# Kernel optimization log

Hardware: AMD Instinct MI355X
Metric: run time of the kernel (lower is better)

Reference implementation:

```python
import jax, jax.numpy as jnp
import numpy as np

B, S, D, N, NC = 2, 1024, 1024, 8192, 8


def _srw_chunked(x, h, emb_norm, tau_offset, w_read, w_write, n_chunks):
    Bd, Sd, Dd = x.shape
    Nd = emb_norm.shape[0]
    cs = Nd // n_chunks
    h_bf = h.astype(jnp.bfloat16)
    x_bf = x.astype(jnp.bfloat16)
    emb_bf = emb_norm.astype(jnp.bfloat16)
    read_bf = w_read.astype(jnp.bfloat16)
    write_bf = w_write.astype(jnp.bfloat16)
    z1 = jnp.zeros((Bd, Sd, 1))

    @jax.checkpoint
    def estimate_stats(h, emb, nc_val):
        ec0 = jax.lax.dynamic_slice_in_dim(emb, 0, cs, axis=0)
        sc0 = h @ ec0.T
        s_sum = sc0.sum(axis=-1, keepdims=True).astype(jnp.float32) * nc_val
        sq_sum = (sc0 ** 2).sum(axis=-1, keepdims=True).astype(jnp.float32) * nc_val
        return (s_sum, sq_sum)

    s_sum, sq_sum = estimate_stats(h_bf, emb_bf, n_chunks)
    s_mean = s_sum / Nd
    s_std = jnp.sqrt(sq_sum / Nd - s_mean ** 2) + 1e-08
    tau = s_mean + tau_offset * s_std
    tau_bf = tau.astype(jnp.bfloat16)

    @jax.checkpoint
    def gsrw_step(carry, i):
        out, es, em, ac, lbs, lbq = carry
        s = i * cs
        ec = jax.lax.dynamic_slice_in_dim(emb_bf, s, cs, axis=0)
        rc = jax.lax.dynamic_slice_in_dim(read_bf, s, cs, axis=0)
        wc = jax.lax.dynamic_slice_in_dim(write_bf, s, cs, axis=0)
        sc = h_bf @ ec.T  # [B,S,cs]
        raw = sc - tau_bf
        gc = jnp.where(raw > 0, raw, (1e-06 * jnp.exp(jnp.clip(raw.astype(jnp.float32), -10.0, 0.0))).astype(jnp.bfloat16))
        gc = jnp.clip(gc, 0.0, 10.0)
        eg = (jnp.exp(gc.astype(jnp.float32)) - 1.0).astype(jnp.bfloat16)
        ef = eg.astype(jnp.float32)
        xr = x_bf @ rc.T  # [B,S,cs]
        co = ((eg * xr) @ wc).astype(jnp.float32)  # [B,S,D]
        gn = ef.mean(axis=(0, 1))
        lbs = lbs + gn.sum()
        lbq = lbq + (gn ** 2).sum()
        return ((out + co,
                 es + ef.sum(axis=-1, keepdims=True),
                 jnp.maximum(em, ef.max(axis=-1, keepdims=True)),
                 ac + (raw > 0).sum(axis=-1, keepdims=True).astype(jnp.float32),
                 lbs, lbq), None)

    z_scalar = jnp.float32(0.0)
    init = (jnp.zeros((Bd, Sd, Dd), dtype=jnp.float32), z1,
            jnp.full((Bd, Sd, 1), -1000000000.0), z1, z_scalar, z_scalar)
    (raw_out, tes, tem, tac, lb_sum, lb_sq), _ = jax.lax.scan(gsrw_step, init, jnp.arange(n_chunks))
    inv_es = (1.0 / (tes + 1e-08)).astype(jnp.bfloat16)
    gs = jnp.tanh(tem).astype(jnp.bfloat16)
    out = raw_out * inv_es * gs
    exp_sum_scalar = tes.mean() + 1e-08
    norm_lb_sum = lb_sum / exp_sum_scalar
    norm_lb_sq = lb_sq / exp_sum_scalar ** 2
    lb_loss = norm_lb_sq * Nd - 2.0 * norm_lb_sum + 1.0
    gs_mean = jnp.tanh(tem).mean()
    es_mean = tes.mean()
    return (out.astype(jnp.float32), tac / Nd, tem, lb_loss, gs_mean, es_mean)


def setup_inputs() -> dict:
    key = jax.random.key(0)
    k = jax.random.split(key, 6)
    x = jax.random.normal(k[0], (B, S, D), jnp.float32)
    h = jax.random.normal(k[1], (B, S, D), jnp.float32)
    emb = jax.random.normal(k[2], (N, D), jnp.float32) * 0.02
    w_read = jax.random.normal(k[3], (N, D), jnp.float32) * 0.02
    w_write = jax.random.normal(k[4], (N, D), jnp.float32) * 0.02
    tau_offset = jax.random.normal(k[5], (B, S, 1), jnp.float32) * 0.1
    return {"x": x, "h": h, "emb": emb, "tau_offset": tau_offset,
            "w_read": w_read, "w_write": w_write, "n_chunks": NC}


def reference(x, h, emb, tau_offset, w_read, w_write, n_chunks):
    # caller (_know_forward) unit-normalizes the embedding pool first
    emb_norm = emb / (jnp.linalg.norm(emb, axis=-1, keepdims=True) + 1e-08)
    out, active_frac, gate_max, lb_loss, gs_mean, es_mean = _srw_chunked(
        x, h, emb_norm, tau_offset, w_read, w_write, n_chunks)
    return out
```

## Files before the change

kernel.cpp:

```cpp
#include <hip/hip_runtime.h>


#define MDIM 2048
#define DDIM 1024
#define NDIM 8192

typedef __attribute__((ext_vector_type(8))) __bf16 bf16x8;
typedef __attribute__((ext_vector_type(4))) float f32x4;

static __device__ __forceinline__ unsigned short f2b(float f) {
  unsigned u = __float_as_uint(f);
  u = (u + 0x7FFFu + ((u >> 16) & 1u)) >> 16;
  return (unsigned short)u;
}
static __device__ __forceinline__ float b2f(unsigned short s) {
  return __uint_as_float(((unsigned)s) << 16);
}

#define LDSF(off) (*(const bf16x8*)(lds + (off)))
#define MFMA_BF16 __builtin_amdgcn_mfma_f32_16x16x32_bf16

#define GLOAD_LDS(gp, lp)                                                              \
  __builtin_amdgcn_global_load_lds(                                                    \
      (const __attribute__((address_space(1))) unsigned int*)(const void*)(gp),        \
      (__attribute__((address_space(3))) unsigned int*)(void*)(lp), 16, 0, 0)

static __device__ __forceinline__ void stage_half(const unsigned short* __restrict__ src,
                                                  int ld, int row0, int k0,
                                                  char* lds, int lds_off, int w, int l) {
  const int rsub = l >> 3;
  const int col = k0 + 8 * ((l & 7) ^ rsub);
#pragma unroll
  for (int j = 0; j < 2; ++j) {
    const unsigned short* g =
        src + (size_t)(row0 + w * 8 + j * 64 + rsub) * (size_t)ld + col;
    GLOAD_LDS(g, lds + lds_off + j * 8192 + w * 1024);
  }
}

static __device__ __forceinline__ void stage4(const unsigned short* __restrict__ asrc,
                                              const unsigned short* __restrict__ bsrc,
                                              int ld, int m0, int n0, int k0,
                                              char* lds, int buf, int w, int l) {
  stage_half(asrc, ld, m0,       k0, lds, buf,         w, l);
  stage_half(asrc, ld, m0 + 128, k0, lds, buf + 16384, w, l);
  stage_half(bsrc, ld, n0,       k0, lds, buf + 32768, w, l);
  stage_half(bsrc, ld, n0 + 128, k0, lds, buf + 49152, w, l);
}

static __device__ __forceinline__ void gemm256(const unsigned short* __restrict__ asrc,
                                               const unsigned short* __restrict__ bsrc,
                                               int ld, int m0, int n0, int kbase,
                                               char* lds, f32x4 (&acc)[8][4],
                                               int w, int l, int wr, int wc) {
  const int lrow = l & 15, lk = l >> 4;
  const int axor = (l & 7) << 4;
  const int kx0 = (lk << 4) ^ axor;
  const int kx1 = (64 | (lk << 4)) ^ axor;
  const int arow_off = lrow * 128;
  const int brow_off = ((wc & 1) * 64 + lrow) * 128;

  stage4(asrc, bsrc, ld, m0, n0, kbase, lds, 0, w, l);
  asm volatile("s_waitcnt vmcnt(0)" ::: "memory");
  __builtin_amdgcn_s_barrier();

#pragma unroll 1
  for (int t = 0; t < 16; ++t) {
    const int buf = (t & 1) * 65536;
    const int nbuf = 65536 - buf;
    if (t < 15) stage4(asrc, bsrc, ld, m0, n0, kbase + (t + 1) * 64, lds, nbuf, w, l);

    const int ab = buf + wr * 16384;
    const int bb = buf + 32768 + (wc >> 1) * 16384;
    bf16x8 aLO[4][2], aHI[4][2], bLO[2][2], bHI[2][2];
#pragma unroll
    for (int m = 0; m < 4; ++m) {
      aLO[m][0] = LDSF(ab + arow_off + m * 2048 + kx0);
      aLO[m][1] = LDSF(ab + arow_off + m * 2048 + kx1);
    }
#pragma unroll
    for (int n = 0; n < 2; ++n) {
      bLO[n][0] = LDSF(bb + brow_off + n * 2048 + kx0);
      bLO[n][1] = LDSF(bb + brow_off + n * 2048 + kx1);
      bHI[n][0] = LDSF(bb + brow_off + (n + 2) * 2048 + kx0);
      bHI[n][1] = LDSF(bb + brow_off + (n + 2) * 2048 + kx1);
    }
    asm volatile("s_waitcnt lgkmcnt(0)" ::: "memory");
    __builtin_amdgcn_s_setprio(1);
#pragma unroll
    for (int ks = 0; ks < 2; ++ks)
#pragma unroll
      for (int n = 0; n < 2; ++n)
#pragma unroll
        for (int m = 0; m < 4; ++m)
          acc[m][n] = MFMA_BF16(aLO[m][ks], bLO[n][ks], acc[m][n], 0, 0, 0);
    __builtin_amdgcn_s_setprio(0);
#pragma unroll
    for (int m = 0; m < 4; ++m) {
      aHI[m][0] = LDSF(ab + arow_off + (m + 4) * 2048 + kx0);
      aHI[m][1] = LDSF(ab + arow_off + (m + 4) * 2048 + kx1);
    }
    __builtin_amdgcn_s_setprio(1);
#pragma unroll
    for (int ks = 0; ks < 2; ++ks)
#pragma unroll
      for (int n = 0; n < 2; ++n)
#pragma unroll
        for (int m = 0; m < 4; ++m)
          acc[m][n + 2] = MFMA_BF16(aLO[m][ks], bHI[n][ks], acc[m][n + 2], 0, 0, 0);
    __builtin_amdgcn_s_setprio(0);
    asm volatile("s_waitcnt lgkmcnt(0)" ::: "memory");
    __builtin_amdgcn_s_setprio(1);
#pragma unroll
    for (int ks = 0; ks < 2; ++ks)
#pragma unroll
      for (int n = 0; n < 2; ++n)
#pragma unroll
        for (int m = 0; m < 4; ++m)
          acc[m + 4][n + 2] = MFMA_BF16(aHI[m][ks], bHI[n][ks], acc[m + 4][n + 2], 0, 0, 0);
#pragma unroll
    for (int ks = 0; ks < 2; ++ks)
#pragma unroll
      for (int n = 0; n < 2; ++n)
#pragma unroll
        for (int m = 0; m < 4; ++m)
          acc[m + 4][n] = MFMA_BF16(aHI[m][ks], bLO[n][ks], acc[m + 4][n], 0, 0, 0);
    __builtin_amdgcn_s_setprio(0);
    asm volatile("s_waitcnt vmcnt(0)" ::: "memory");
    __builtin_amdgcn_s_barrier();
  }
}


__global__ __launch_bounds__(256) void k_prep(const float* __restrict__ emb,
                                              const float* __restrict__ w_read,
                                              const float* __restrict__ h,
                                              const float* __restrict__ x,
                                              const float* __restrict__ w_write,
                                              unsigned short* __restrict__ eb,
                                              unsigned short* __restrict__ rb,
                                              unsigned short* __restrict__ hb,
                                              unsigned short* __restrict__ xb,
                                              unsigned short* __restrict__ wbT) {
  const int b = blockIdx.x, t = threadIdx.x;
  if (b < 2048) {
    __shared__ float tsm[64][65];
    const int nb = b & 127, db = b >> 7;
    const int r = t >> 2, c4 = (t & 3) * 16;
#pragma unroll
    for (int j = 0; j < 4; ++j) {
      const float4 v = *(const float4*)&w_write[(size_t)(nb * 64 + r) * 1024 + db * 64 + c4 + 4 * j];
      tsm[r][c4 + 4 * j + 0] = v.x;
      tsm[r][c4 + 4 * j + 1] = v.y;
      tsm[r][c4 + 4 * j + 2] = v.z;
      tsm[r][c4 + 4 * j + 3] = v.w;
    }
    __syncthreads();
    const int dr = t >> 2, nc0 = (t & 3) * 16;
    unsigned pk[8];
#pragma unroll
    for (int j = 0; j < 8; ++j) {
      const unsigned lo = f2b(tsm[nc0 + 2 * j][dr]);
      const unsigned hi = f2b(tsm[nc0 + 2 * j + 1][dr]);
      pk[j] = lo | (hi << 16);
    }
    uint4* dst = (uint4*)(wbT + (size_t)(db * 64 + dr) * 8192 + nb * 64 + nc0);
    uint4 w0, w1;
    w0.x = pk[0]; w0.y = pk[1]; w0.z = pk[2]; w0.w = pk[3];
    w1.x = pk[4]; w1.y = pk[5]; w1.z = pk[6]; w1.w = pk[7];
    dst[0] = w0;
    dst[1] = w1;
  } else if (b < 10240) {
    const int n = b - 2048;
    const float4 v = ((const float4*)(emb + (size_t)n * 1024))[t];
    float ss = v.x * v.x + v.y * v.y + v.z * v.z + v.w * v.w;
#pragma unroll
    for (int off = 1; off < 64; off <<= 1) ss += __shfl_xor(ss, off, 64);
    __shared__ float wsum[4];
    if ((t & 63) == 0) wsum[t >> 6] = ss;
    __syncthreads();
    const float denom = sqrtf(wsum[0] + wsum[1] + wsum[2] + wsum[3]) + 1e-8f;
    ushort4 o;
    o.x = f2b(v.x / denom);
    o.y = f2b(v.y / denom);
    o.z = f2b(v.z / denom);
    o.w = f2b(v.w / denom);
    ((ushort4*)(eb + (size_t)n * 1024))[t] = o;
  } else {
    const float* src;
    unsigned short* dst;
    int i;
    if (b < 18432) { src = w_read; dst = rb; i = (b - 10240) * 256 + t; }
    else if (b < 20480) { src = h; dst = hb; i = (b - 18432) * 256 + t; }
    else { src = x; dst = xb; i = (b - 20480) * 256 + t; }
    const float4 v = ((const float4*)src)[i];
    ushort4 o;
    o.x = f2b(v.x);
    o.y = f2b(v.y);
    o.z = f2b(v.z);
    o.w = f2b(v.w);
    ((ushort4*)dst)[i] = o;
  }
}


template <int TROWS>
static __device__ __forceinline__ void stage_tile(const unsigned short* __restrict__ src,
                                                  int row0, int k0, int ld,
                                                  unsigned short* lds, int wave, int lane) {
  const int rsub = lane >> 3;
  const int csub = (lane & 7) << 3;
#pragma unroll
  for (int q = 0; q < TROWS / 32; ++q) {
    const int p = q * 4 + wave;
    const unsigned short* g =
        src + (size_t)(row0 + p * 8 + rsub) * (size_t)ld + (size_t)(k0 + csub);
    GLOAD_LDS(g, lds + p * 512);
  }
}

__global__ __launch_bounds__(256, 2) void k_stats(const unsigned short* __restrict__ hb,
                                                  const unsigned short* __restrict__ eb,
                                                  float* __restrict__ stat_s,
                                                  float* __restrict__ stat_q) {
  __shared__ unsigned short a_sm[64 * 64];
  __shared__ unsigned short b_sm[128 * 64];
  __shared__ float red_s[2][64];
  __shared__ float red_q[2][64];
  const int t = threadIdx.x;
  const int wave = t >> 6, lane = t & 63;
  const int wr = wave >> 1, wc = wave & 1;
  const int m0 = blockIdx.x * 64, n0 = blockIdx.y * 128;
  const int arow = lane & 15;
  const int kcol = (lane >> 4) << 3;
  f32x4 acc[2][4];
#pragma unroll
  for (int m = 0; m < 2; ++m)
#pragma unroll
    for (int n = 0; n < 4; ++n) acc[m][n] = (f32x4)0.0f;
  for (int k0 = 0; k0 < 1024; k0 += 64) {
    stage_tile<64>(hb, m0, k0, 1024, a_sm, wave, lane);
    stage_tile<128>(eb, n0, k0, 1024, b_sm, wave, lane);
    asm volatile("s_waitcnt vmcnt(0)" ::: "memory");
    __syncthreads();
#pragma unroll
    for (int ks = 0; ks < 2; ++ks) {
      bf16x8 af[2], bfr[4];
#pragma unroll
      for (int m = 0; m < 2; ++m)
        af[m] = *(const bf16x8*)&a_sm[(wr * 32 + m * 16 + arow) * 64 + ks * 32 + kcol];
#pragma unroll
      for (int n = 0; n < 4; ++n)
        bfr[n] = *(const bf16x8*)&b_sm[(wc * 64 + n * 16 + arow) * 64 + ks * 32 + kcol];
#pragma unroll
      for (int m = 0; m < 2; ++m)
#pragma unroll
        for (int n = 0; n < 4; ++n)
          acc[m][n] = MFMA_BF16(af[m], bfr[n], acc[m][n], 0, 0, 0);
    }
    __syncthreads();
  }

  float s_r[2][4], q_r[2][4];
#pragma unroll
  for (int m = 0; m < 2; ++m)
#pragma unroll
    for (int i = 0; i < 4; ++i) { s_r[m][i] = 0.f; q_r[m][i] = 0.f; }
#pragma unroll
  for (int m = 0; m < 2; ++m)
#pragma unroll
    for (int n = 0; n < 4; ++n)
#pragma unroll
      for (int i = 0; i < 4; ++i) {
        const float scf = b2f(f2b(acc[m][n][i]));
        s_r[m][i] += scf;
        q_r[m][i] += b2f(f2b(scf * scf));
      }
#pragma unroll
  for (int m = 0; m < 2; ++m)
#pragma unroll
    for (int i = 0; i < 4; ++i) {
      float s = s_r[m][i], q = q_r[m][i];
      for (int off = 1; off < 16; off <<= 1) {
        s += __shfl_xor(s, off, 64);
        q += __shfl_xor(q, off, 64);
      }
      if ((lane & 15) == 0) {
        const int rloc = wr * 32 + m * 16 + (lane >> 4) * 4 + i;
        red_s[wc][rloc] = s;
        red_q[wc][rloc] = q;
      }
    }
  __syncthreads();
  if (t < 64) {
    stat_s[(size_t)(m0 + t) * 8 + blockIdx.y] = red_s[0][t] + red_s[1][t];
    stat_q[(size_t)(m0 + t) * 8 + blockIdx.y] = red_q[0][t] + red_q[1][t];
  }
}

__global__ void k_tau(const float* __restrict__ stat_s, const float* __restrict__ stat_q,
                      const float* __restrict__ tau_off, float* __restrict__ tau) {
  const int r = blockIdx.x * 256 + threadIdx.x;
  if (r >= MDIM) return;
  float S = 0.f, Q = 0.f;
#pragma unroll
  for (int j = 0; j < 8; ++j) {
    S += stat_s[(size_t)r * 8 + j];
    Q += stat_q[(size_t)r * 8 + j];
  }
  const float s_sum = S * 8.0f;
  const float sq_sum = Q * 8.0f;
  const float mean = s_sum * (1.0f / 8192.0f);
  const float var = __fsub_rn(sq_sum * (1.0f / 8192.0f), __fmul_rn(mean, mean));
  const float sd = __fadd_rn(__fsqrt_rn(var), 1e-8f);
  const float tv = __fadd_rn(mean, __fmul_rn(tau_off[r], sd));
  tau[r] = b2f(f2b(tv));
}


__global__ __launch_bounds__(512, 2) void k_sc(const unsigned short* __restrict__ hb,
                                               const unsigned short* __restrict__ eb,
                                               const float* __restrict__ tau,
                                               unsigned short* __restrict__ Aeg,
                                               float* __restrict__ es_part,
                                               float* __restrict__ em_part) {
  __shared__ __align__(16) char lds[131072];
  const int t = threadIdx.x, w = t >> 6, l = t & 63;
  const int wr = w >> 2, wc = w & 3;
  const int bid = blockIdx.x;
  const int swz = (bid & 7) * 32 + (bid >> 3);
  const int m0 = (swz >> 5) * 256, n0 = (swz & 31) * 256;
  f32x4 acc[8][4];
#pragma unroll
  for (int m = 0; m < 8; ++m)
#pragma unroll
    for (int n = 0; n < 4; ++n) acc[m][n] = (f32x4)0.0f;
  gemm256(hb, eb, 1024, m0, n0, 0, lds, acc, w, l, wr, wc);

  __syncthreads();
  float* tau_sm = (float*)lds;
  float* red_es = (float*)(lds + 1024);
  float* red_em = (float*)(lds + 1024 + 4096);
  if (t < 256) tau_sm[t] = tau[m0 + t];
  __syncthreads();
  const int lrow = l & 15, lk = l >> 4;
#pragma unroll
  for (int m = 0; m < 8; ++m) {
#pragma unroll
    for (int i = 0; i < 4; ++i) {
      const int rl = wr * 128 + m * 16 + lk * 4 + i;
      const float taub = tau_sm[rl];
      float es_v = 0.f, em_v = 0.f;
#pragma unroll
      for (int n = 0; n < 4; ++n) {
        const float scf = b2f(f2b(acc[m][n][i]));
        const float rawf = b2f(f2b(scf - taub));
        float gcf;
        if (rawf > 0.f) gcf = fminf(rawf, 10.0f);
        else gcf = b2f(f2b(1e-6f * expf(fmaxf(rawf, -10.0f))));
        const unsigned short egu = f2b(expf(gcf) - 1.0f);
        const float ef = b2f(egu);
        es_v += ef;
        em_v = fmaxf(em_v, ef);
        Aeg[(size_t)(m0 + rl) * NDIM + (size_t)(n0 + wc * 64 + n * 16 + lrow)] = egu;
      }
      for (int off = 1; off < 16; off <<= 1) {
        es_v += __shfl_xor(es_v, off, 64);
        em_v = fmaxf(em_v, __shfl_xor(em_v, off, 64));
      }
      if (lrow == 0) {
        red_es[wc * 256 + rl] = es_v;
        red_em[wc * 256 + rl] = em_v;
      }
    }
  }
  __syncthreads();
  if (t < 256) {
    const float s = red_es[t] + red_es[256 + t] + red_es[512 + t] + red_es[768 + t];
    const float e = fmaxf(fmaxf(red_em[t], red_em[256 + t]),
                          fmaxf(red_em[512 + t], red_em[768 + t]));
    es_part[(size_t)(m0 + t) * 32 + (n0 >> 8)] = s;
    em_part[(size_t)(m0 + t) * 32 + (n0 >> 8)] = e;
  }
}


__global__ __launch_bounds__(512, 2) void k_xr(const unsigned short* __restrict__ xb,
                                               const unsigned short* __restrict__ rb,
                                               unsigned short* __restrict__ Aeg) {
  __shared__ __align__(16) char lds[131072];
  const int t = threadIdx.x, w = t >> 6, l = t & 63;
  const int wr = w >> 2, wc = w & 3;
  const int bid = blockIdx.x;
  const int swz = (bid & 7) * 32 + (bid >> 3);
  const int m0 = (swz >> 5) * 256, n0 = (swz & 31) * 256;
  f32x4 acc[8][4];
#pragma unroll
  for (int m = 0; m < 8; ++m)
#pragma unroll
    for (int n = 0; n < 4; ++n) acc[m][n] = (f32x4)0.0f;
  gemm256(xb, rb, 1024, m0, n0, 0, lds, acc, w, l, wr, wc);

  const int lrow = l & 15, lk = l >> 4;
#pragma unroll
  for (int m = 0; m < 8; ++m)
#pragma unroll
    for (int n = 0; n < 4; ++n)
#pragma unroll
      for (int i = 0; i < 4; ++i) {
        const int rl = wr * 128 + m * 16 + lk * 4 + i;
        const size_t idx =
            (size_t)(m0 + rl) * NDIM + (size_t)(n0 + wc * 64 + n * 16 + lrow);
        const unsigned short egu = Aeg[idx];
        const float xrf = b2f(f2b(acc[m][n][i]));
        Aeg[idx] = f2b(b2f(egu) * xrf);
      }
}


__global__ __launch_bounds__(512, 2) void k_out(const unsigned short* __restrict__ A,
                                                const unsigned short* __restrict__ wbT,
                                                unsigned short* __restrict__ pacc) {
  __shared__ __align__(16) char lds[131072];
  const int t = threadIdx.x, w = t >> 6, l = t & 63;
  const int wr = w >> 2, wc = w & 3;
  const int bid = blockIdx.x;
  const int swz = (bid & 7) * 32 + (bid >> 3);
  const int bm = swz >> 5, chunk = (swz >> 2) & 7, bd = swz & 3;
  const int m0 = bm * 256, d0 = bd * 256;
  f32x4 acc[8][4];
#pragma unroll
  for (int m = 0; m < 8; ++m)
#pragma unroll
    for (int n = 0; n < 4; ++n) acc[m][n] = (f32x4)0.0f;
  gemm256(A, wbT, 8192, m0, d0, chunk * 1024, lds, acc, w, l, wr, wc);

  const int lrow = l & 15, lk = l >> 4;
#pragma unroll
  for (int m = 0; m < 8; ++m)
#pragma unroll
    for (int n = 0; n < 4; ++n)
#pragma unroll
      for (int i = 0; i < 4; ++i) {
        const int rl = wr * 128 + m * 16 + lk * 4 + i;
        pacc[((size_t)chunk * MDIM + (m0 + rl)) * DDIM +
             (size_t)(d0 + wc * 64 + n * 16 + lrow)] = f2b(acc[m][n][i]);
      }
}


__global__ void k_scale(const float* __restrict__ es_part, const float* __restrict__ em_part,
                        float* __restrict__ scale2) {
  const int r = blockIdx.x * 256 + threadIdx.x;
  if (r >= MDIM) return;
  float s = 0.f, m = 0.f;
#pragma unroll
  for (int j = 0; j < 32; ++j) {
    s += es_part[(size_t)r * 32 + j];
    m = fmaxf(m, em_part[(size_t)r * 32 + j]);
  }
  scale2[2 * r] = b2f(f2b(1.0f / (s + 1e-8f)));
  scale2[2 * r + 1] = b2f(f2b(tanhf(m)));
}

__global__ __launch_bounds__(256) void k_finish(const unsigned short* __restrict__ pacc,
                                                const float* __restrict__ scale2,
                                                float* __restrict__ outp) {
  const int t = blockIdx.x * 256 + threadIdx.x;
  const int r = t >> 8;
  const int d4 = (t & 255) * 4;
  float sx = 0.f, sy = 0.f, sz = 0.f, sw = 0.f;
#pragma unroll
  for (int c = 0; c < 8; ++c) {
    const ushort4 v = *(const ushort4*)(pacc + ((size_t)c * MDIM + r) * DDIM + d4);
    sx += b2f(v.x);
    sy += b2f(v.y);
    sz += b2f(v.z);
    sw += b2f(v.w);
  }
  const float inv = scale2[2 * r];
  const float gsv = scale2[2 * r + 1];
  float4 o;
  o.x = (sx * inv) * gsv;
  o.y = (sy * inv) * gsv;
  o.z = (sz * inv) * gsv;
  o.w = (sw * inv) * gsv;
  *(float4*)(outp + (size_t)r * DDIM + d4) = o;
}


extern "C" void kernel_launch(void* const* d_in, const int* in_sizes, int n_in,
                              void* d_out, int out_size, void* d_ws, size_t ws_size,
                              hipStream_t stream) {
  const float* x = (const float*)d_in[0];
  const float* h = (const float*)d_in[1];
  const float* emb = (const float*)d_in[2];
  const float* tau_off = (const float*)d_in[3];
  const float* w_read = (const float*)d_in[4];
  const float* w_write = (const float*)d_in[5];

  char* ws = (char*)d_ws;
  const size_t MB = 1024 * 1024;
  unsigned short* rb = (unsigned short*)(ws);
  unsigned short* eb = (unsigned short*)(ws + 16 * MB);
  unsigned short* wbT = (unsigned short*)(ws + 32 * MB);
  unsigned short* hb = (unsigned short*)(ws + 48 * MB);
  unsigned short* xb = (unsigned short*)(ws + 52 * MB);
  unsigned short* Aeg = (unsigned short*)(ws + 56 * MB);
  unsigned short* pacc = (unsigned short*)(ws);
  float* tau = (float*)(ws + 88 * MB);
  float* stat_s = (float*)(ws + 88 * MB + 1 * 65536);
  float* stat_q = (float*)(ws + 88 * MB + 2 * 65536);
  float* es_part = (float*)(ws + 88 * MB + 3 * 65536);
  float* em_part = (float*)(ws + 88 * MB + 7 * 65536);
  float* scale2 = (float*)(ws + 88 * MB + 11 * 65536);
  if (ws_size < 88 * MB + 12 * 65536) return;
  float* outp = (float*)d_out;

  k_prep<<<22528, 256, 0, stream>>>(emb, w_read, h, x, w_write, eb, rb, hb, xb, wbT);
  k_stats<<<dim3(MDIM / 64, 8), 256, 0, stream>>>(hb, eb, stat_s, stat_q);
  k_tau<<<MDIM / 256, 256, 0, stream>>>(stat_s, stat_q, tau_off, tau);
  k_sc<<<256, 512, 0, stream>>>(hb, eb, tau, Aeg, es_part, em_part);
  k_scale<<<MDIM / 256, 256, 0, stream>>>(es_part, em_part, scale2);
  k_xr<<<256, 512, 0, stream>>>(xb, rb, Aeg);
  k_out<<<256, 512, 0, stream>>>(Aeg, wbT, pacc);
  k_finish<<<(MDIM * DDIM / 4) / 256, 256, 0, stream>>>(pacc, scale2, outp);
}
```

Before: 190.6 us.

## Fuse gate and read-projection GEMMs into one kernel keeping gates in registers

Merges the score/gate kernel and the x·read kernel into a single kernel that runs both 256x256 GEMMs back to back. The gate values are packed into registers instead of being written to the Aeg buffer and read back, which removes one full round trip of the 2048x8192 bf16 intermediate through global memory and one kernel launch. In exchange it adds 64 packed registers per thread while the accumulators are live, which risks spills at launch bounds of 2 blocks per CU. It also moves tau and the reduction scratch out of the 128 KB LDS buffer into separate shared arrays, raising total LDS per block.

```diff
diff --git a/kernel.cpp b/kernel.cpp
--- a/kernel.cpp
+++ b/kernel.cpp
@@ -318,18 +318,25 @@
 }
 
 
-__global__ __launch_bounds__(512, 2) void k_sc(const unsigned short* __restrict__ hb,
-                                               const unsigned short* __restrict__ eb,
-                                               const float* __restrict__ tau,
-                                               unsigned short* __restrict__ Aeg,
-                                               float* __restrict__ es_part,
-                                               float* __restrict__ em_part) {
+__global__ __launch_bounds__(512, 2) void k_gate(const unsigned short* __restrict__ hb,
+                                                 const unsigned short* __restrict__ eb,
+                                                 const unsigned short* __restrict__ xb,
+                                                 const unsigned short* __restrict__ rb,
+                                                 const float* __restrict__ tau,
+                                                 unsigned short* __restrict__ Aeg,
+                                                 float* __restrict__ es_part,
+                                                 float* __restrict__ em_part) {
   __shared__ __align__(16) char lds[131072];
+  __shared__ float tau_sm[256];
+  __shared__ float red_es[1024];
+  __shared__ float red_em[1024];
   const int t = threadIdx.x, w = t >> 6, l = t & 63;
   const int wr = w >> 2, wc = w & 3;
   const int bid = blockIdx.x;
   const int swz = (bid & 7) * 32 + (bid >> 3);
   const int m0 = (swz >> 5) * 256, n0 = (swz & 31) * 256;
+  const int lrow = l & 15, lk = l >> 4;
+
   f32x4 acc[8][4];
 #pragma unroll
   for (int m = 0; m < 8; ++m)
@@ -338,12 +345,9 @@
   gemm256(hb, eb, 1024, m0, n0, 0, lds, acc, w, l, wr, wc);
 
   __syncthreads();
-  float* tau_sm = (float*)lds;
-  float* red_es = (float*)(lds + 1024);
-  float* red_em = (float*)(lds + 1024 + 4096);
   if (t < 256) tau_sm[t] = tau[m0 + t];
   __syncthreads();
-  const int lrow = l & 15, lk = l >> 4;
+  unsigned eg_pk[8][4][2];
 #pragma unroll
   for (int m = 0; m < 8; ++m) {
 #pragma unroll
@@ -351,6 +355,7 @@
       const int rl = wr * 128 + m * 16 + lk * 4 + i;
       const float taub = tau_sm[rl];
       float es_v = 0.f, em_v = 0.f;
+      unsigned p0 = 0, p1 = 0;
 #pragma unroll
       for (int n = 0; n < 4; ++n) {
         const float scf = b2f(f2b(acc[m][n][i]));
@@ -362,8 +367,11 @@
         const float ef = b2f(egu);
         es_v += ef;
         em_v = fmaxf(em_v, ef);
-        Aeg[(size_t)(m0 + rl) * NDIM + (size_t)(n0 + wc * 64 + n * 16 + lrow)] = egu;
-      }
+        if (n < 2) p0 |= ((unsigned)egu) << (16 * n);
+        else       p1 |= ((unsigned)egu) << (16 * (n - 2));
+      }
+      eg_pk[m][i][0] = p0;
+      eg_pk[m][i][1] = p1;
       for (int off = 1; off < 16; off <<= 1) {
         es_v += __shfl_xor(es_v, off, 64);
         em_v = fmaxf(em_v, __shfl_xor(em_v, off, 64));
@@ -382,26 +390,13 @@
     es_part[(size_t)(m0 + t) * 32 + (n0 >> 8)] = s;
     em_part[(size_t)(m0 + t) * 32 + (n0 >> 8)] = e;
   }
-}
-
-
-__global__ __launch_bounds__(512, 2) void k_xr(const unsigned short* __restrict__ xb,
-                                               const unsigned short* __restrict__ rb,
-                                               unsigned short* __restrict__ Aeg) {
-  __shared__ __align__(16) char lds[131072];
-  const int t = threadIdx.x, w = t >> 6, l = t & 63;
-  const int wr = w >> 2, wc = w & 3;
-  const int bid = blockIdx.x;
-  const int swz = (bid & 7) * 32 + (bid >> 3);
-  const int m0 = (swz >> 5) * 256, n0 = (swz & 31) * 256;
-  f32x4 acc[8][4];
+
 #pragma unroll
   for (int m = 0; m < 8; ++m)
 #pragma unroll
     for (int n = 0; n < 4; ++n) acc[m][n] = (f32x4)0.0f;
   gemm256(xb, rb, 1024, m0, n0, 0, lds, acc, w, l, wr, wc);
 
-  const int lrow = l & 15, lk = l >> 4;
 #pragma unroll
   for (int m = 0; m < 8; ++m)
 #pragma unroll
@@ -409,11 +404,11 @@
 #pragma unroll
       for (int i = 0; i < 4; ++i) {
         const int rl = wr * 128 + m * 16 + lk * 4 + i;
-        const size_t idx =
-            (size_t)(m0 + rl) * NDIM + (size_t)(n0 + wc * 64 + n * 16 + lrow);
-        const unsigned short egu = Aeg[idx];
+        const unsigned short egu =
+            (unsigned short)((eg_pk[m][i][n >> 1] >> (16 * (n & 1))) & 0xFFFFu);
         const float xrf = b2f(f2b(acc[m][n][i]));
-        Aeg[idx] = f2b(b2f(egu) * xrf);
+        Aeg[(size_t)(m0 + rl) * NDIM + (size_t)(n0 + wc * 64 + n * 16 + lrow)] =
+            f2b(b2f(egu) * xrf);
       }
 }
 
@@ -520,9 +515,8 @@
   k_prep<<<22528, 256, 0, stream>>>(emb, w_read, h, x, w_write, eb, rb, hb, xb, wbT);
   k_stats<<<dim3(MDIM / 64, 8), 256, 0, stream>>>(hb, eb, stat_s, stat_q);
   k_tau<<<MDIM / 256, 256, 0, stream>>>(stat_s, stat_q, tau_off, tau);
-  k_sc<<<256, 512, 0, stream>>>(hb, eb, tau, Aeg, es_part, em_part);
+  k_gate<<<256, 512, 0, stream>>>(hb, eb, xb, rb, tau, Aeg, es_part, em_part);
   k_scale<<<MDIM / 256, 256, 0, stream>>>(es_part, em_part, scale2);
-  k_xr<<<256, 512, 0, stream>>>(xb, rb, Aeg);
   k_out<<<256, 512, 0, stream>>>(Aeg, wbT, pacc);
   k_finish<<<(MDIM * DDIM / 4) / 256, 256, 0, stream>>>(pacc, scale2, outp);
 }
```

New measurement: 236.7 us. 1.24x slower.
